# Kernel tuning notes

Hardware: AMD Instinct MI355X
Metric: run time of the kernel (lower is better)

The kernel has to match this reference:

```python
import jax, jax.numpy as jnp
import numpy as np

N = 2048      # feature_num (nodes/sensors)
T = 5         # timd_num (window length)
D = 64        # embed_dim
TOPK = 21     # topk + 1 (includes self, cos(i,i)=1)
B = 32        # batch
EPS = 1e-5
NEG_SLOPE = 0.2


def setup_inputs() -> dict:
    key = jax.random.key(0)
    ks = jax.random.split(key, 9)
    s = 1.0 / np.sqrt(D)
    return {
        "x": jax.random.normal(ks[0], (B, N, T), jnp.float32),
        "emb": jax.random.normal(ks[1], (N, D), jnp.float32) * s,      # embedding table
        "W": jax.random.normal(ks[2], (D, T), jnp.float32) * (1.0 / np.sqrt(T)),  # GNN lin weight
        "Wb": jax.random.normal(ks[3], (D,), jnp.float32) * 0.01,       # GNN lin bias
        "a_src": jax.random.normal(ks[4], (2 * D,), jnp.float32) * s,   # attention vec (source half)
        "a_dst": jax.random.normal(ks[5], (2 * D,), jnp.float32) * s,   # attention vec (dest half)
        "gamma": jnp.ones((D,), jnp.float32),                            # BatchNorm1d weight
        "beta": jnp.zeros((D,), jnp.float32),                            # BatchNorm1d bias
        "fc_w": jax.random.normal(ks[6], (1, D), jnp.float32) * s,      # fc weight
        "fc_b": jnp.zeros((1,), jnp.float32),                            # fc bias
    }


def reference(x, emb, W, Wb, a_src, a_dst, gamma, beta, fc_w, fc_b):
    # --- cosine-sim topk graph build ---
    norm = jnp.linalg.norm(emb, axis=-1)                    # [N]
    cos = (emb @ emb.T) / (norm[:, None] * norm[None, :])   # [N,N]
    _, idx = jax.lax.top_k(cos, TOPK)                       # [N,TOPK]
    # scatter one-hot adjacency (vectorized, no per-row loop)
    adj = jnp.zeros((N, N), x.dtype).at[jnp.arange(N)[:, None], idx].set(1.0)
    # --- GNN: GDN-style attention message passing ---
    h = jnp.einsum('bnt,dt->bnd', x, W) + Wb                # [B,N,D]
    g = jnp.concatenate([h, jnp.broadcast_to(emb, h.shape)], axis=-1)  # [B,N,2D]
    e_src = g @ a_src                                       # [B,N]
    e_dst = g @ a_dst                                       # [B,N]
    e = jax.nn.leaky_relu(e_src[:, :, None] + e_dst[:, None, :], NEG_SLOPE)  # [B,N,N]
    e = jnp.where(adj > 0, e, jnp.float32(-1e9))
    alpha = jax.nn.softmax(e, axis=-1)                      # [B,N,N], rows sum to 1 over TOPK nbrs
    z = jax.nn.relu(jnp.einsum('bij,bjd->bid', alpha, h))   # [B,N,D]
    # --- output head: z * emb, BN over channels, relu, fc ---
    out = z * emb                                           # [B,N,D]
    mean = out.mean(axis=(0, 1))                            # BN1d stats over (batch, nodes)
    var = out.var(axis=(0, 1))
    out = (out - mean) * jax.lax.rsqrt(var + EPS) * gamma + beta
    out = jax.nn.relu(out)
    out = out @ fc_w.T + fc_b                               # [B,N,1]
    return out.reshape(-1, N)                               # [B,N]
```

## Files before the change

kernel.cpp:

```cpp
#include <hip/hip_runtime.h>
#include <math.h>

#define N_NODES 2048
#define T_WIN 5
#define D_EMB 64
#define TOPK 21
#define B_BATCH 32
#define BN_TOTAL (B_BATCH * N_NODES)
#define EPS_BN 1e-5f
#define NEG_SLOPE 0.2f
#define STATS_STRIDE 16

typedef unsigned long long u64;

__device__ __forceinline__ float wave_sum(float v) {
#pragma unroll
    for (int off = 32; off > 0; off >>= 1) v += __shfl_xor(v, off, 64);
    return v;
}

__device__ __forceinline__ u64 max64(u64 a, u64 b) { return a > b ? a : b; }
__device__ __forceinline__ u64 min64(u64 a, u64 b) { return a < b ? a : b; }

__device__ __forceinline__ u64 bitonic_sort64_desc(u64 key, int lane) {
#pragma unroll
    for (int k = 2; k <= 64; k <<= 1) {
#pragma unroll
        for (int j = k >> 1; j >= 1; j >>= 1) {
            u64 pk = __shfl_xor(key, j, 64);
            bool dirDesc = ((lane & k) == 0);
            bool keepMax = (((lane & j) == 0) == dirDesc);
            key = keepMax ? max64(key, pk) : min64(key, pk);
        }
    }
    return key;
}

__device__ __forceinline__ u64 bitonic_merge_top64(u64 a, u64 b, int lane) {
    u64 br = __shfl(b, 63 - lane, 64);
    u64 c = max64(a, br);
#pragma unroll
    for (int j = 32; j >= 1; j >>= 1) {
        u64 pk = __shfl_xor(c, j, 64);
        bool keepMax = ((lane & j) == 0);
        c = keepMax ? max64(c, pk) : min64(c, pk);
    }
    return c;
}

__global__ __launch_bounds__(256) void k_pre(
    const float* __restrict__ x, const float* __restrict__ W,
    const float* __restrict__ Wb, const float* __restrict__ a_src,
    const float* __restrict__ a_dst, const float* __restrict__ emb,
    float* __restrict__ xs2T, float* __restrict__ xd2T,
    float* __restrict__ es_embP, float* __restrict__ ed_embP,
    float* __restrict__ norms, float* __restrict__ stats,
    float* __restrict__ stats2) {
    int t = threadIdx.x;
    if (blockIdx.x < 512) {
        if (blockIdx.x < 2) {
            float* p = blockIdx.x ? stats2 : stats;
            ((float4*)p)[t] = make_float4(0.f, 0.f, 0.f, 0.f);
        }
        int wid = t >> 6, lane = t & 63;
        int node = blockIdx.x * 4 + wid;
        float e = emb[node * D_EMB + lane];
        float s2 = wave_sum(e * e);
        float esE = wave_sum(e * a_src[D_EMB + lane]);
        float edE = wave_sum(e * a_dst[D_EMB + lane]);
        if (lane == 0) {
            norms[node] = sqrtf(s2);
            es_embP[node] = esE;
            ed_embP[node] = edE;
        }
        return;
    }

    __shared__ float cws[5], cwd[5], cbs[2];
    if (t < 12) {
        int which = (t < 5 || t == 10) ? 0 : 1;
        const float* av = which ? a_dst : a_src;
        const float* sp;
        int stride;
        if (t < 10) { int tt = (t < 5) ? t : t - 5; sp = W + tt; stride = T_WIN; }
        else        { sp = Wb; stride = 1; }
        float acc = 0.f;
        for (int d = 0; d < D_EMB; d++) acc += sp[d * stride] * av[d];
        if (t < 5)       cws[t] = acc;
        else if (t < 10) cwd[t - 5] = acc;
        else             cbs[t - 10] = acc;
    }
    __syncthreads();
    float ws0 = cws[0], ws1 = cws[1], ws2 = cws[2], ws3 = cws[3], ws4 = cws[4];
    float wd0 = cwd[0], wd1 = cwd[1], wd2 = cwd[2], wd3 = cwd[3], wd4 = cwd[4];
    float bss = cbs[0], bsd = cbs[1];

    int base = (blockIdx.x - 512) * 1024;
#pragma unroll
    for (int r = 0; r < 4; r++) {
        int item = base + 256 * r + t;
        const float* xp = x + (size_t)item * T_WIN;
        float x0 = xp[0], x1 = xp[1], x2 = xp[2], x3 = xp[3], x4 = xp[4];
        xs2T[item] = bss + x0 * ws0 + x1 * ws1 + x2 * ws2 + x3 * ws3 + x4 * ws4;
        xd2T[item] = bsd + x0 * wd0 + x1 * wd1 + x2 * wd2 + x3 * wd3 + x4 * wd4;
    }
}

__global__ __launch_bounds__(256) void k_gram(
    const float* __restrict__ emb, const float* __restrict__ norms,
    float* __restrict__ cosM) {
    __shared__ __align__(16) float As[64][68];
    __shared__ __align__(16) float Bs[64][68];
    int t = threadIdx.x;
    int g = blockIdx.x;
    int a = (int)((sqrtf(8.f * g + 1.f) - 1.f) * 0.5f);
    while ((a + 1) * (a + 2) / 2 <= g) a++;
    while (a * (a + 1) / 2 > g) a--;
    int bq = g - a * (a + 1) / 2;
    int i0 = a * 64, j0 = bq * 64;

    {
        int r = t >> 2, c0 = t & 3;
        const float4* srcA = (const float4*)(emb + (size_t)(i0 + r) * D_EMB);
        const float4* srcB = (const float4*)(emb + (size_t)(j0 + r) * D_EMB);
#pragma unroll
        for (int k = 0; k < 4; k++) {
            int f4 = c0 + 4 * k;
            float4 v = srcA[f4];
            int d = 4 * f4;
            As[d][r] = v.x; As[d + 1][r] = v.y; As[d + 2][r] = v.z; As[d + 3][r] = v.w;
            float4 w = srcB[f4];
            Bs[d][r] = w.x; Bs[d + 1][r] = w.y; Bs[d + 2][r] = w.z; Bs[d + 3][r] = w.w;
        }
    }
    __syncthreads();

    int ti = t & 15, tj = t >> 4;
    float acc[4][4] = {};
#pragma unroll
    for (int d = 0; d < 64; d++) {
        float4 av = *(const float4*)&As[d][4 * ti];
        float4 bv = *(const float4*)&Bs[d][4 * tj];
        acc[0][0] += av.x * bv.x; acc[0][1] += av.x * bv.y; acc[0][2] += av.x * bv.z; acc[0][3] += av.x * bv.w;
        acc[1][0] += av.y * bv.x; acc[1][1] += av.y * bv.y; acc[1][2] += av.y * bv.z; acc[1][3] += av.y * bv.w;
        acc[2][0] += av.z * bv.x; acc[2][1] += av.z * bv.y; acc[2][2] += av.z * bv.z; acc[2][3] += av.z * bv.w;
        acc[3][0] += av.w * bv.x; acc[3][1] += av.w * bv.y; acc[3][2] += av.w * bv.z; acc[3][3] += av.w * bv.w;
    }

    float nis[4] = {norms[i0 + 4 * ti], norms[i0 + 4 * ti + 1],
                    norms[i0 + 4 * ti + 2], norms[i0 + 4 * ti + 3]};
    float njs[4] = {norms[j0 + 4 * tj], norms[j0 + 4 * tj + 1],
                    norms[j0 + 4 * tj + 2], norms[j0 + 4 * tj + 3]};
#pragma unroll
    for (int r = 0; r < 4; r++) {
        float4 o;
        o.x = acc[r][0] / (nis[r] * njs[0]);
        o.y = acc[r][1] / (nis[r] * njs[1]);
        o.z = acc[r][2] / (nis[r] * njs[2]);
        o.w = acc[r][3] / (nis[r] * njs[3]);
        int i = i0 + 4 * ti + r;
        *(float4*)(cosM + (size_t)i * N_NODES + j0 + 4 * tj) = o;
        cosM[(size_t)(j0 + 4 * tj + 0) * N_NODES + i] = o.x;
        cosM[(size_t)(j0 + 4 * tj + 1) * N_NODES + i] = o.y;
        cosM[(size_t)(j0 + 4 * tj + 2) * N_NODES + i] = o.z;
        cosM[(size_t)(j0 + 4 * tj + 3) * N_NODES + i] = o.w;
    }
}

__global__ __launch_bounds__(256) void k_select(
    const float* __restrict__ cosM, int* __restrict__ idxT) {
    __shared__ u64 candbuf[4][128];
    __shared__ u64 mbuf[2][64];
    int tid = threadIdx.x;
    int wid = tid >> 6, lane = tid & 63;
    int pair = wid >> 1;
    int half = wid & 1;
    int i = blockIdx.x * 2 + pair;
    int jbase = half * (N_NODES / 2);
    const float* row = cosM + (size_t)i * N_NODES + jbase;
    u64* buf = candbuf[wid];

    u64 a = 0;
    u64 t = 0;
    int cnt = 0;
    float vcur = row[lane];

#pragma unroll 1
    for (int c = 0; c < N_NODES / 128; c++) {
        int j = c * 64 + lane;
        float v = vcur;
        if (c < N_NODES / 128 - 1) vcur = row[j + 64];
        unsigned u = __float_as_uint(v);
        u = (u & 0x80000000u) ? ~u : (u | 0x80000000u);
        u64 key = ((u64)u << 32) | (unsigned)(~(j + jbase));
        unsigned long long ball = __ballot(key > t);
        if (ball) {
            int ofs = __popcll(ball & ((1ull << lane) - 1ull));
            if (key > t) buf[cnt + ofs] = key;
            cnt += (int)__popcll(ball);
            if (cnt >= 64) {
                u64 nk = buf[lane];
                nk = bitonic_sort64_desc(nk, lane);
                a = bitonic_merge_top64(a, nk, lane);
                t = __shfl(a, 20, 64);
                int rem = cnt - 64;
                u64 mv = (lane < rem) ? buf[64 + lane] : 0;
                if (lane < rem) buf[lane] = mv;
                cnt = rem;
            }
        }
    }
    while (cnt > 0) {
        int take = cnt < 64 ? cnt : 64;
        u64 nk = (lane < take) ? buf[lane] : 0;
        nk = bitonic_sort64_desc(nk, lane);
        a = bitonic_merge_top64(a, nk, lane);
        t = __shfl(a, 20, 64);
        int rem = cnt - take;
        u64 mv = (lane < rem) ? buf[take + lane] : 0;
        if (lane < rem) buf[lane] = mv;
        cnt = rem;
    }

    if (half) mbuf[pair][lane] = a;
    __syncthreads();
    if (!half) {
        u64 bv = mbuf[pair][lane];
        a = bitonic_merge_top64(a, bv, lane);
        if (lane < TOPK) idxT[lane * N_NODES + i] = (int)(~(unsigned)a);
    }
}

__global__ __launch_bounds__(256) void k_alpha(
    const int* __restrict__ idxT, const float* __restrict__ xs2T,
    const float* __restrict__ xd2T, const float* __restrict__ es_embP,
    const float* __restrict__ ed_embP, float* __restrict__ alphaT) {
    __shared__ float sed[N_NODES];
    int g = blockIdx.x;
    int b = g & 31;
    int i0 = (g >> 5) * 256;
    int t = threadIdx.x;

    {
        const float4* sxd = (const float4*)(xd2T + (size_t)b * N_NODES);
        const float4* sde = (const float4*)(ed_embP);
        float4* dst = (float4*)sed;
#pragma unroll
        for (int q = 0; q < 2; q++) {
            int idx = t + 256 * q;
            float4 u = sxd[idx];
            float4 v = sde[idx];
            dst[idx] = make_float4(u.x + v.x, u.y + v.y, u.z + v.z, u.w + v.w);
        }
    }
    __syncthreads();

    int i = i0 + t;
    float es = xs2T[(size_t)b * N_NODES + i] + es_embP[i];
    float ev[TOPK];
    float m = -3e38f;
#pragma unroll
    for (int k = 0; k < TOPK; k++) {
        int jk = idxT[k * N_NODES + i];
        float e = es + sed[jk];
        e = e > 0.f ? e : NEG_SLOPE * e;
        ev[k] = e;
        m = fmaxf(m, e);
    }
    float s = 0.f;
#pragma unroll
    for (int k = 0; k < TOPK; k++) {
        ev[k] = __expf(ev[k] - m);
        s += ev[k];
    }
    float inv = 1.0f / s;
#pragma unroll
    for (int k = 0; k < TOPK; k++)
        alphaT[((size_t)b * TOPK + k) * N_NODES + i] = ev[k] * inv;
}

__global__ __launch_bounds__(256, 2) void k_msg(
    const float* __restrict__ x, const float* __restrict__ W,
    const float* __restrict__ Wb, const int* __restrict__ idxT,
    const float* __restrict__ alphaT, const float* __restrict__ emb,
    float* __restrict__ obufT, float* __restrict__ stats,
    float* __restrict__ stats2) {
    __shared__ float hts[N_NODES][6];
    __shared__ float sred[2][4][4];

    int g = blockIdx.x;
    int b = (g & 7) + 8 * ((g >> 3) & 3);
    int c = g >> 5;
    int d0 = c * 4;
    int t = threadIdx.x;
    int wid = t >> 6, lane = t & 63;

    float wc[4][T_WIN], wb4[4];
#pragma unroll
    for (int q = 0; q < 4; q++) {
        wb4[q] = Wb[d0 + q];
#pragma unroll
        for (int tt = 0; tt < T_WIN; tt++) wc[q][tt] = W[(d0 + q) * T_WIN + tt];
    }
    const float* xb = x + (size_t)b * N_NODES * T_WIN;
#pragma unroll
    for (int r = 0; r < 8; r++) {
        int row = t + 256 * r;
        const float* xr = xb + row * T_WIN;
        float x0 = xr[0], x1 = xr[1], x2 = xr[2], x3 = xr[3], x4 = xr[4];
        float h0 = wb4[0] + x0 * wc[0][0] + x1 * wc[0][1] + x2 * wc[0][2] + x3 * wc[0][3] + x4 * wc[0][4];
        float h1 = wb4[1] + x0 * wc[1][0] + x1 * wc[1][1] + x2 * wc[1][2] + x3 * wc[1][3] + x4 * wc[1][4];
        float h2 = wb4[2] + x0 * wc[2][0] + x1 * wc[2][1] + x2 * wc[2][2] + x3 * wc[2][3] + x4 * wc[2][4];
        float h3 = wb4[3] + x0 * wc[3][0] + x1 * wc[3][1] + x2 * wc[3][2] + x3 * wc[3][3] + x4 * wc[3][4];
        *(float2*)&hts[row][0] = make_float2(h0, h1);
        *(float2*)&hts[row][2] = make_float2(h2, h3);
    }
    __syncthreads();

    float sacc[4] = {0.f, 0.f, 0.f, 0.f};
    float sacc2[4] = {0.f, 0.f, 0.f, 0.f};
    const float* aT = alphaT + (size_t)b * TOPK * N_NODES;
#pragma unroll 1
    for (int r = 0; r < 8; r++) {
        int i = 256 * r + t;
        float4 z = make_float4(0.f, 0.f, 0.f, 0.f);
#pragma unroll
        for (int k = 0; k < TOPK; k++) {
            int jk = idxT[k * N_NODES + i];
            float a = aT[(size_t)k * N_NODES + i];
            float2 h01 = *(const float2*)&hts[jk][0];
            float2 h23 = *(const float2*)&hts[jk][2];
            z.x = fmaf(a, h01.x, z.x);
            z.y = fmaf(a, h01.y, z.y);
            z.z = fmaf(a, h23.x, z.z);
            z.w = fmaf(a, h23.y, z.w);
        }
        float4 e4 = *(const float4*)(emb + (size_t)i * D_EMB + d0);
        float4 o;
        o.x = fmaxf(z.x, 0.f) * e4.x;
        o.y = fmaxf(z.y, 0.f) * e4.y;
        o.z = fmaxf(z.z, 0.f) * e4.z;
        o.w = fmaxf(z.w, 0.f) * e4.w;
        ((float4*)obufT)[((size_t)c * B_BATCH + b) * N_NODES + i] = o;
        sacc[0] += o.x; sacc[1] += o.y; sacc[2] += o.z; sacc[3] += o.w;
        sacc2[0] += o.x * o.x; sacc2[1] += o.y * o.y;
        sacc2[2] += o.z * o.z; sacc2[3] += o.w * o.w;
    }

#pragma unroll
    for (int q = 0; q < 4; q++) {
        sacc[q] = wave_sum(sacc[q]);
        sacc2[q] = wave_sum(sacc2[q]);
    }
    if (lane == 0) {
#pragma unroll
        for (int q = 0; q < 4; q++) {
            sred[0][wid][q] = sacc[q];
            sred[1][wid][q] = sacc2[q];
        }
    }
    __syncthreads();
    if (t < 8) {
        int q = t & 3, which = t >> 2;
        float v = sred[which][0][q] + sred[which][1][q] + sred[which][2][q] + sred[which][3][q];
        float* dst = which ? stats2 : stats;
        atomicAdd(&dst[(d0 + q) * STATS_STRIDE], v);
    }
}

__global__ __launch_bounds__(256) void k_out(
    const float* __restrict__ obufT, const float* __restrict__ stats,
    const float* __restrict__ stats2, const float* __restrict__ gamma,
    const float* __restrict__ beta, const float* __restrict__ fc_w,
    const float* __restrict__ fc_b, float* __restrict__ out) {
    __shared__ float smean[64], sinv[64], sg[64], sb[64], sf[64];
    int t = threadIdx.x;
    int g = blockIdx.x;
    int b = g & 31, nc = g >> 5;
    int n = nc * 256 + t;
    const float invM = 1.0f / (float)BN_TOTAL;

    if (t < 64) {
        float mn = stats[t * STATS_STRIDE] * invM;
        float var = stats2[t * STATS_STRIDE] * invM - mn * mn;
        smean[t] = mn;
        sinv[t] = rsqrtf(var + EPS_BN);
        sg[t] = gamma[t]; sb[t] = beta[t]; sf[t] = fc_w[t];
    }
    __syncthreads();

    float fb = fc_b[0];
    float p = 0.f;
#pragma unroll
    for (int c = 0; c < 16; c++) {
        float4 o = ((const float4*)obufT)[((size_t)c * B_BATCH + b) * N_NODES + n];
        int d = 4 * c;
        float v;
        v = fmaxf((o.x - smean[d + 0]) * sinv[d + 0] * sg[d + 0] + sb[d + 0], 0.f); p = fmaf(v, sf[d + 0], p);
        v = fmaxf((o.y - smean[d + 1]) * sinv[d + 1] * sg[d + 1] + sb[d + 1], 0.f); p = fmaf(v, sf[d + 1], p);
        v = fmaxf((o.z - smean[d + 2]) * sinv[d + 2] * sg[d + 2] + sb[d + 2], 0.f); p = fmaf(v, sf[d + 2], p);
        v = fmaxf((o.w - smean[d + 3]) * sinv[d + 3] * sg[d + 3] + sb[d + 3], 0.f); p = fmaf(v, sf[d + 3], p);
    }
    out[b * N_NODES + n] = p + fb;
}

extern "C" void kernel_launch(void* const* d_in, const int* in_sizes, int n_in,
                              void* d_out, int out_size, void* d_ws, size_t ws_size,
                              hipStream_t stream) {
    const float* x     = (const float*)d_in[0];
    const float* emb   = (const float*)d_in[1];
    const float* W     = (const float*)d_in[2];
    const float* Wb    = (const float*)d_in[3];
    const float* a_src = (const float*)d_in[4];
    const float* a_dst = (const float*)d_in[5];
    const float* gamma = (const float*)d_in[6];
    const float* beta  = (const float*)d_in[7];
    const float* fc_w  = (const float*)d_in[8];
    const float* fc_b  = (const float*)d_in[9];
    float* out = (float*)d_out;

    char* ws = (char*)d_ws;
    float* stats   = (float*)(ws + 0);
    float* stats2  = (float*)(ws + 4096);
    int*   idxT    = (int*)  (ws + 8192);
    float* norms   = (float*)(ws + 180224);
    float* es_embP = (float*)(ws + 188416);
    float* ed_embP = (float*)(ws + 196608);
    float* xs2T    = (float*)(ws + 204800);
    float* xd2T    = (float*)(ws + 466944);
    float* alphaT  = (float*)(ws + 729088);
    float* cosM    = (float*)(ws + 6234112);
    float* obufT   = cosM;

    k_pre<<<576, 256, 0, stream>>>(x, W, Wb, a_src, a_dst, emb,
                                   xs2T, xd2T, es_embP, ed_embP, norms,
                                   stats, stats2);
    k_gram<<<528, 256, 0, stream>>>(emb, norms, cosM);
    k_select<<<N_NODES / 2, 256, 0, stream>>>(cosM, idxT);
    k_alpha<<<256, 256, 0, stream>>>(idxT, xs2T, xd2T, es_embP, ed_embP, alphaT);
    k_msg<<<512, 256, 0, stream>>>(x, W, Wb, idxT, alphaT, emb, obufT, stats, stats2);
    k_out<<<256, 256, 0, stream>>>(obufT, stats, stats2, gamma, beta, fc_w, fc_b, out);
}
```

Measured before the change: 137.1 us.

## Fuse preprocessing into gram kernel, defer cosine normalization to select

Merges the preprocessing kernel into the gram kernel as extra blocks, so one launch and one dependency are removed. The gram kernel now stores raw dot products, and the select kernel divides by the norms on the fly, which removes the gram kernel's dependency on norms. The message kernel packs h into float4 rows, shrinking shared memory, and raises its occupancy hint to 4 blocks per CU. The fused kernel's grid is heterogeneous, and the select kernel now loads norms and divides for every element.

```diff
diff --git a/kernel.cpp b/kernel.cpp
--- a/kernel.cpp
+++ b/kernel.cpp
@@ -48,70 +48,68 @@
     return c;
 }
 
-__global__ __launch_bounds__(256) void k_pre(
+__global__ __launch_bounds__(256) void k_preg(
     const float* __restrict__ x, const float* __restrict__ W,
     const float* __restrict__ Wb, const float* __restrict__ a_src,
     const float* __restrict__ a_dst, const float* __restrict__ emb,
     float* __restrict__ xs2T, float* __restrict__ xd2T,
     float* __restrict__ es_embP, float* __restrict__ ed_embP,
-    float* __restrict__ norms, float* __restrict__ stats,
-    float* __restrict__ stats2) {
-    int t = threadIdx.x;
-    if (blockIdx.x < 512) {
-        if (blockIdx.x < 2) {
-            float* p = blockIdx.x ? stats2 : stats;
-            ((float4*)p)[t] = make_float4(0.f, 0.f, 0.f, 0.f);
-        }
-        int wid = t >> 6, lane = t & 63;
-        int node = blockIdx.x * 4 + wid;
-        float e = emb[node * D_EMB + lane];
-        float s2 = wave_sum(e * e);
-        float esE = wave_sum(e * a_src[D_EMB + lane]);
-        float edE = wave_sum(e * a_dst[D_EMB + lane]);
-        if (lane == 0) {
-            norms[node] = sqrtf(s2);
-            es_embP[node] = esE;
-            ed_embP[node] = edE;
-        }
-        return;
-    }
-
-    __shared__ float cws[5], cwd[5], cbs[2];
-    if (t < 12) {
-        int which = (t < 5 || t == 10) ? 0 : 1;
-        const float* av = which ? a_dst : a_src;
-        const float* sp;
-        int stride;
-        if (t < 10) { int tt = (t < 5) ? t : t - 5; sp = W + tt; stride = T_WIN; }
-        else        { sp = Wb; stride = 1; }
-        float acc = 0.f;
-        for (int d = 0; d < D_EMB; d++) acc += sp[d * stride] * av[d];
-        if (t < 5)       cws[t] = acc;
-        else if (t < 10) cwd[t - 5] = acc;
-        else             cbs[t - 10] = acc;
-    }
-    __syncthreads();
-    float ws0 = cws[0], ws1 = cws[1], ws2 = cws[2], ws3 = cws[3], ws4 = cws[4];
-    float wd0 = cwd[0], wd1 = cwd[1], wd2 = cwd[2], wd3 = cwd[3], wd4 = cwd[4];
-    float bss = cbs[0], bsd = cbs[1];
-
-    int base = (blockIdx.x - 512) * 1024;
-#pragma unroll
-    for (int r = 0; r < 4; r++) {
-        int item = base + 256 * r + t;
-        const float* xp = x + (size_t)item * T_WIN;
-        float x0 = xp[0], x1 = xp[1], x2 = xp[2], x3 = xp[3], x4 = xp[4];
-        xs2T[item] = bss + x0 * ws0 + x1 * ws1 + x2 * ws2 + x3 * ws3 + x4 * ws4;
-        xd2T[item] = bsd + x0 * wd0 + x1 * wd1 + x2 * wd2 + x3 * wd3 + x4 * wd4;
-    }
-}
-
-__global__ __launch_bounds__(256) void k_gram(
-    const float* __restrict__ emb, const float* __restrict__ norms,
-    float* __restrict__ cosM) {
+    float* __restrict__ norms, float* __restrict__ dotM,
+    float* __restrict__ stats, float* __restrict__ stats2) {
     __shared__ __align__(16) float As[64][68];
     __shared__ __align__(16) float Bs[64][68];
     int t = threadIdx.x;
+
+    if (blockIdx.x >= 528) {
+        int eb = blockIdx.x - 528;
+        if (eb < 512) {
+            if (eb < 2) {
+                float* p = eb ? stats2 : stats;
+                ((float4*)p)[t] = make_float4(0.f, 0.f, 0.f, 0.f);
+            }
+            int wid = t >> 6, lane = t & 63;
+            int node = eb * 4 + wid;
+            float e = emb[node * D_EMB + lane];
+            float s2 = wave_sum(e * e);
+            float esE = wave_sum(e * a_src[D_EMB + lane]);
+            float edE = wave_sum(e * a_dst[D_EMB + lane]);
+            if (lane == 0) {
+                norms[node] = sqrtf(s2);
+                es_embP[node] = esE;
+                ed_embP[node] = edE;
+            }
+        } else {
+            __shared__ float cws[5], cwd[5], cbs[2];
+            if (t < 12) {
+                int which = (t < 5 || t == 10) ? 0 : 1;
+                const float* av = which ? a_dst : a_src;
+                const float* sp;
+                int stride;
+                if (t < 10) { int tt = (t < 5) ? t : t - 5; sp = W + tt; stride = T_WIN; }
+                else        { sp = Wb; stride = 1; }
+                float acc = 0.f;
+                for (int d = 0; d < D_EMB; d++) acc += sp[d * stride] * av[d];
+                if (t < 5)       cws[t] = acc;
+                else if (t < 10) cwd[t - 5] = acc;
+                else             cbs[t - 10] = acc;
+            }
+            __syncthreads();
+            float ws0 = cws[0], ws1 = cws[1], ws2 = cws[2], ws3 = cws[3], ws4 = cws[4];
+            float wd0 = cwd[0], wd1 = cwd[1], wd2 = cwd[2], wd3 = cwd[3], wd4 = cwd[4];
+            float bss = cbs[0], bsd = cbs[1];
+            int base = (eb - 512) * 1024;
+#pragma unroll
+            for (int r = 0; r < 4; r++) {
+                int item = base + 256 * r + t;
+                const float* xp = x + (size_t)item * T_WIN;
+                float x0 = xp[0], x1 = xp[1], x2 = xp[2], x3 = xp[3], x4 = xp[4];
+                xs2T[item] = bss + x0 * ws0 + x1 * ws1 + x2 * ws2 + x3 * ws3 + x4 * ws4;
+                xd2T[item] = bsd + x0 * wd0 + x1 * wd1 + x2 * wd2 + x3 * wd3 + x4 * wd4;
+            }
+        }
+        return;
+    }
+
     int g = blockIdx.x;
     int a = (int)((sqrtf(8.f * g + 1.f) - 1.f) * 0.5f);
     while ((a + 1) * (a + 2) / 2 <= g) a++;
@@ -147,28 +145,22 @@
         acc[3][0] += av.w * bv.x; acc[3][1] += av.w * bv.y; acc[3][2] += av.w * bv.z; acc[3][3] += av.w * bv.w;
     }
 
-    float nis[4] = {norms[i0 + 4 * ti], norms[i0 + 4 * ti + 1],
-                    norms[i0 + 4 * ti + 2], norms[i0 + 4 * ti + 3]};
-    float njs[4] = {norms[j0 + 4 * tj], norms[j0 + 4 * tj + 1],
-                    norms[j0 + 4 * tj + 2], norms[j0 + 4 * tj + 3]};
 #pragma unroll
     for (int r = 0; r < 4; r++) {
         float4 o;
-        o.x = acc[r][0] / (nis[r] * njs[0]);
-        o.y = acc[r][1] / (nis[r] * njs[1]);
-        o.z = acc[r][2] / (nis[r] * njs[2]);
-        o.w = acc[r][3] / (nis[r] * njs[3]);
+        o.x = acc[r][0]; o.y = acc[r][1]; o.z = acc[r][2]; o.w = acc[r][3];
         int i = i0 + 4 * ti + r;
-        *(float4*)(cosM + (size_t)i * N_NODES + j0 + 4 * tj) = o;
-        cosM[(size_t)(j0 + 4 * tj + 0) * N_NODES + i] = o.x;
-        cosM[(size_t)(j0 + 4 * tj + 1) * N_NODES + i] = o.y;
-        cosM[(size_t)(j0 + 4 * tj + 2) * N_NODES + i] = o.z;
-        cosM[(size_t)(j0 + 4 * tj + 3) * N_NODES + i] = o.w;
+        *(float4*)(dotM + (size_t)i * N_NODES + j0 + 4 * tj) = o;
+        dotM[(size_t)(j0 + 4 * tj + 0) * N_NODES + i] = o.x;
+        dotM[(size_t)(j0 + 4 * tj + 1) * N_NODES + i] = o.y;
+        dotM[(size_t)(j0 + 4 * tj + 2) * N_NODES + i] = o.z;
+        dotM[(size_t)(j0 + 4 * tj + 3) * N_NODES + i] = o.w;
     }
 }
 
 __global__ __launch_bounds__(256) void k_select(
-    const float* __restrict__ cosM, int* __restrict__ idxT) {
+    const float* __restrict__ dotM, const float* __restrict__ norms,
+    int* __restrict__ idxT) {
     __shared__ u64 candbuf[4][128];
     __shared__ u64 mbuf[2][64];
     int tid = threadIdx.x;
@@ -177,19 +169,25 @@
     int half = wid & 1;
     int i = blockIdx.x * 2 + pair;
     int jbase = half * (N_NODES / 2);
-    const float* row = cosM + (size_t)i * N_NODES + jbase;
+    const float* row = dotM + (size_t)i * N_NODES + jbase;
     u64* buf = candbuf[wid];
+    float ni = norms[i];
 
     u64 a = 0;
     u64 t = 0;
     int cnt = 0;
     float vcur = row[lane];
+    float ncur = norms[jbase + lane];
 
 #pragma unroll 1
     for (int c = 0; c < N_NODES / 128; c++) {
         int j = c * 64 + lane;
-        float v = vcur;
-        if (c < N_NODES / 128 - 1) vcur = row[j + 64];
+        float dv = vcur, nv = ncur;
+        if (c < N_NODES / 128 - 1) {
+            vcur = row[j + 64];
+            ncur = norms[jbase + j + 64];
+        }
+        float v = dv / (ni * nv);
         unsigned u = __float_as_uint(v);
         u = (u & 0x80000000u) ? ~u : (u | 0x80000000u);
         u64 key = ((u64)u << 32) | (unsigned)(~(j + jbase));
@@ -279,13 +277,13 @@
         alphaT[((size_t)b * TOPK + k) * N_NODES + i] = ev[k] * inv;
 }
 
-__global__ __launch_bounds__(256, 2) void k_msg(
+__global__ __launch_bounds__(256, 4) void k_msg(
     const float* __restrict__ x, const float* __restrict__ W,
     const float* __restrict__ Wb, const int* __restrict__ idxT,
     const float* __restrict__ alphaT, const float* __restrict__ emb,
     float* __restrict__ obufT, float* __restrict__ stats,
     float* __restrict__ stats2) {
-    __shared__ float hts[N_NODES][6];
+    __shared__ __align__(16) float hts[N_NODES][4];
     __shared__ float sred[2][4][4];
 
     int g = blockIdx.x;
@@ -312,8 +310,7 @@
         float h1 = wb4[1] + x0 * wc[1][0] + x1 * wc[1][1] + x2 * wc[1][2] + x3 * wc[1][3] + x4 * wc[1][4];
         float h2 = wb4[2] + x0 * wc[2][0] + x1 * wc[2][1] + x2 * wc[2][2] + x3 * wc[2][3] + x4 * wc[2][4];
         float h3 = wb4[3] + x0 * wc[3][0] + x1 * wc[3][1] + x2 * wc[3][2] + x3 * wc[3][3] + x4 * wc[3][4];
-        *(float2*)&hts[row][0] = make_float2(h0, h1);
-        *(float2*)&hts[row][2] = make_float2(h2, h3);
+        *(float4*)&hts[row][0] = make_float4(h0, h1, h2, h3);
     }
     __syncthreads();
 
@@ -328,12 +325,11 @@
         for (int k = 0; k < TOPK; k++) {
             int jk = idxT[k * N_NODES + i];
             float a = aT[(size_t)k * N_NODES + i];
-            float2 h01 = *(const float2*)&hts[jk][0];
-            float2 h23 = *(const float2*)&hts[jk][2];
-            z.x = fmaf(a, h01.x, z.x);
-            z.y = fmaf(a, h01.y, z.y);
-            z.z = fmaf(a, h23.x, z.z);
-            z.w = fmaf(a, h23.y, z.w);
+            float4 h4 = *(const float4*)&hts[jk][0];
+            z.x = fmaf(a, h4.x, z.x);
+            z.y = fmaf(a, h4.y, z.y);
+            z.z = fmaf(a, h4.z, z.z);
+            z.w = fmaf(a, h4.w, z.w);
         }
         float4 e4 = *(const float4*)(emb + (size_t)i * D_EMB + d0);
         float4 o;
@@ -429,14 +425,13 @@
     float* xs2T    = (float*)(ws + 204800);
     float* xd2T    = (float*)(ws + 466944);
     float* alphaT  = (float*)(ws + 729088);
-    float* cosM    = (float*)(ws + 6234112);
-    float* obufT   = cosM;
-
-    k_pre<<<576, 256, 0, stream>>>(x, W, Wb, a_src, a_dst, emb,
-                                   xs2T, xd2T, es_embP, ed_embP, norms,
-                                   stats, stats2);
-    k_gram<<<528, 256, 0, stream>>>(emb, norms, cosM);
-    k_select<<<N_NODES / 2, 256, 0, stream>>>(cosM, idxT);
+    float* dotM    = (float*)(ws + 6234112);
+    float* obufT   = dotM;
+
+    k_preg<<<1104, 256, 0, stream>>>(x, W, Wb, a_src, a_dst, emb,
+                                     xs2T, xd2T, es_embP, ed_embP, norms,
+                                     dotM, stats, stats2);
+    k_select<<<N_NODES / 2, 256, 0, stream>>>(dotM, norms, idxT);
     k_alpha<<<256, 256, 0, stream>>>(idxT, xs2T, xd2T, es_embP, ed_embP, alphaT);
     k_msg<<<512, 256, 0, stream>>>(x, W, Wb, idxT, alphaT, emb, obufT, stats, stats2);
     k_out<<<256, 256, 0, stream>>>(obufT, stats, stats2, gamma, beta, fc_w, fc_b, out);
```

Measured after the change: 131.4 us. -4.1%, faster.
